# Optimization experiments

Measured on AMD Instinct MI355X. Metric: run time of the kernel, lower is better.

The kernel has to match this reference:

```python
import jax, jax.numpy as jnp
import numpy as np

B, C, H, W = 16, 512, 48, 48
INTER = 64  # C // reduction


def setup_inputs() -> dict:
    key = jax.random.key(0)
    k1, k2, k3, k4, k5 = jax.random.split(key, 5)
    s = 0.05
    return {
        "x": jax.random.normal(k1, (B, C, H, W), dtype=jnp.float32),
        "Wq": jax.random.normal(k2, (INTER, C), dtype=jnp.float32) * s,
        "Wk": jax.random.normal(k3, (INTER, C), dtype=jnp.float32) * s,
        "Wv": jax.random.normal(k4, (C, C), dtype=jnp.float32) * s,
        "gamma": jax.random.normal(k5, (1,), dtype=jnp.float32),
    }


def reference(x, Wq, Wk, Wv, gamma):
    b, c, h, w = x.shape
    n = h * w
    xf = x.reshape(b, c, n)                       # (B, C, N)
    # 1x1 convs == channel-mixing GEMMs
    q = jnp.einsum("ic,bcn->bin", Wq, xf)         # (B, inter, N)
    k = jnp.einsum("ic,bcn->bin", Wk, xf)         # (B, inter, N)
    v = jnp.einsum("oc,bcn->bon", Wv, xf)         # (B, C, N)
    # attn[b, n, m] = q[b, :, n] . k[b, :, m]; softmax over m
    attn = jnp.einsum("bin,bim->bnm", q, k)       # (B, N, N)
    attn = jax.nn.softmax(attn, axis=-1)
    # out[b, c, n] = sum_m v[b, c, m] * attn[b, n, m]
    out = jnp.einsum("bcm,bnm->bcn", v, attn).reshape(b, c, h, w)
    return gamma[0] * out + x
```

## Files before the change

### kernel.cpp

```cpp
#include <hip/hip_runtime.h>

#define BATCH 16
#define CHN   512
#define INTER 64
#define NPIX  2304

typedef _Float16 f16;
typedef _Float16 f16x8 __attribute__((ext_vector_type(8)));
typedef _Float16 f16x4 __attribute__((ext_vector_type(4)));
typedef short    s16x8 __attribute__((ext_vector_type(8)));
typedef float    f32x16 __attribute__((ext_vector_type(16)));

#define XT_OFF   ((size_t)0)
#define QT_OFF   ((size_t)37748736)
#define KT_OFF   ((size_t)42467328)
#define VB_OFF   ((size_t)47185920)
#define WHQ_OFF  ((size_t)84934656)
#define WHK_OFF  ((size_t)85000192)
#define WHV_OFF  ((size_t)85065728)

__device__ inline unsigned short f2bf(float f) {
    unsigned int u = __float_as_uint(f);
    unsigned int r = (u + 0x7FFFu + ((u >> 16) & 1u)) >> 16;
    return (unsigned short)r;
}

__device__ inline unsigned pack_bf16(float a, float b) {
    unsigned ua = __float_as_uint(a) + 0x8000u;
    unsigned ub = __float_as_uint(b) + 0x8000u;
    return __builtin_amdgcn_perm(ub, ua, 0x07060302u);
}

__device__ inline void swap32(unsigned x, unsigned y, unsigned& nx, unsigned& ny, int lh) {
#if __has_builtin(__builtin_amdgcn_permlane32_swap)
    auto r = __builtin_amdgcn_permlane32_swap(x, y, false, false);
    nx = r[0]; ny = r[1];
#else
    const unsigned xs = (unsigned)__shfl_xor((int)x, 32, 64);
    const unsigned ys = (unsigned)__shfl_xor((int)y, 32, 64);
    nx = lh ? ys : x;
    ny = lh ? y  : xs;
#endif
}

__global__ __launch_bounds__(256) void convert_x_kernel(
    const float* __restrict__ x, f16* __restrict__ xT)
{
    const int n0 = blockIdx.x * 64;
    const int c0 = blockIdx.y * 64;
    const int b  = blockIdx.z;
    const int t  = threadIdx.x;

    __shared__ float tile[64][65];

    {
        const int cr   = t >> 2;
        const int ncol = (t & 3) * 16;
        const float* src = x + ((size_t)b * CHN + (size_t)(c0 + cr)) * NPIX + n0 + ncol;
        #pragma unroll
        for (int u = 0; u < 4; ++u) {
            const float4 v4 = *(const float4*)(src + u * 4);
            tile[cr][ncol + u * 4 + 0] = v4.x;
            tile[cr][ncol + u * 4 + 1] = v4.y;
            tile[cr][ncol + u * 4 + 2] = v4.z;
            tile[cr][ncol + u * 4 + 3] = v4.w;
        }
    }
    __syncthreads();
    #pragma unroll
    for (int r = 0; r < 2; ++r) {
        const int id = t + r * 256;
        const int n  = id >> 3;
        const int cg = id & 7;
        f16x8 o;
        #pragma unroll
        for (int j = 0; j < 8; ++j) o[j] = (f16)tile[cg * 8 + j][n];
        *(f16x8*)(xT + ((size_t)b * NPIX + (size_t)(n0 + n)) * CHN + c0 + cg * 8) = o;
    }
}

__global__ __launch_bounds__(256) void convert_w_kernel(
    const float* __restrict__ Wq, const float* __restrict__ Wk,
    const float* __restrict__ Wv, f16* __restrict__ whq,
    f16* __restrict__ whk, f16* __restrict__ whv)
{
    const int which = blockIdx.y;
    const float* src; f16* dst; int count;
    if (which == 0)      { src = Wq; dst = whq; count = 64 * 512; }
    else if (which == 1) { src = Wk; dst = whk; count = 64 * 512; }
    else                 { src = Wv; dst = whv; count = 512 * 512; }
    const int i = (blockIdx.x * 256 + threadIdx.x) * 4;
    if (i < count) {
        const float4 v4 = *(const float4*)(src + i);
        f16x4 o;
        o[0] = (f16)v4.x; o[1] = (f16)v4.y; o[2] = (f16)v4.z; o[3] = (f16)v4.w;
        *(f16x4*)(dst + i) = o;
    }
}

__global__ __launch_bounds__(256, 2) void proj_kernel(
    const f16* __restrict__ xT, const f16* __restrict__ whq,
    const f16* __restrict__ whk, const f16* __restrict__ whv,
    f16* __restrict__ qTo, f16* __restrict__ kTo,
    unsigned short* __restrict__ vout)
{
    const int nt = blockIdx.x;
    const int rt = blockIdx.y;
    const int b  = blockIdx.z;
    const int t  = threadIdx.x;
    const int wave = t >> 6, lane = t & 63;
    const int row = lane & 31, lh = lane >> 5;

    __shared__ f16 wsm[128][72];
    __shared__ f16 xs[128][72];

    f32x16 acc[4];
    #pragma unroll
    for (int s = 0; s < 4; ++s)
        #pragma unroll
        for (int r = 0; r < 16; ++r) acc[s][r] = 0.0f;

    for (int c0 = 0; c0 < CHN; c0 += 64) {
        __syncthreads();
        #pragma unroll
        for (int r = 0; r < 4; ++r) {
            const int id = t + r * 256;
            const int co = id >> 3, cg = id & 7;
            const f16* src;
            if (rt == 0) src = (co < 64) ? (whq + (size_t)co * CHN)
                                         : (whk + (size_t)(co - 64) * CHN);
            else         src = whv + (size_t)((rt - 1) * 128 + co) * CHN;
            *(f16x8*)&wsm[co][cg * 8] = *(const f16x8*)(src + c0 + cg * 8);
        }
        #pragma unroll
        for (int r = 0; r < 4; ++r) {
            const int id = t + r * 256;
            const int n = id >> 3, cg = id & 7;
            *(f16x8*)&xs[n][cg * 8] =
                *(const f16x8*)(xT + ((size_t)b * NPIX + (size_t)(nt * 128 + n)) * CHN + c0 + cg * 8);
        }
        __syncthreads();

        #pragma unroll
        for (int kk = 0; kk < 64; kk += 16) {
            const f16x8 bf = *(const f16x8*)&xs[wave * 32 + row][kk + lh * 8];
            #pragma unroll
            for (int cs = 0; cs < 4; ++cs) {
                const f16x8 af = *(const f16x8*)&wsm[cs * 32 + row][kk + lh * 8];
                acc[cs] = __builtin_amdgcn_mfma_f32_32x32x16_f16(af, bf, acc[cs], 0, 0, 0);
            }
        }
    }

    const int n = nt * 128 + wave * 32 + row;
    if (rt == 0) {
        #pragma unroll
        for (int cs = 0; cs < 4; ++cs)
            #pragma unroll
            for (int r = 0; r < 16; ++r) {
                const int i = cs * 32 + (r & 3) + 8 * (r >> 2) + 4 * lh;
                const f16 val = (f16)acc[cs][r];
                if (i < 64) qTo[((size_t)b * NPIX + n) * INTER + i] = val;
                else        kTo[((size_t)b * NPIX + n) * INTER + i - 64] = val;
            }
    } else {
        #pragma unroll
        for (int cs = 0; cs < 4; ++cs)
            #pragma unroll
            for (int r = 0; r < 16; ++r) {
                const int c = (rt - 1) * 128 + cs * 32 + (r & 3) + 8 * (r >> 2) + 4 * lh;
                vout[((size_t)b * CHN + c) * NPIX + n] = f2bf(acc[cs][r]);
            }
    }
}

__global__ __launch_bounds__(256, 3) void attn_kernel(
    const float* __restrict__ x, const float* __restrict__ gamma,
    const f16* __restrict__ qT, const f16* __restrict__ kT,
    const unsigned short* __restrict__ vglob, float* __restrict__ out)
{
    const int nt = blockIdx.x;
    const int cq = blockIdx.y;
    const int b  = blockIdx.z;
    const int t  = threadIdx.x;
    const int wave = t >> 6, lane = t & 63;
    const int row = lane & 31, lh = lane >> 5;

    __shared__ short vbuf[2][128 * 64];
    __shared__ f16   kbuf[2][64 * 64];

    const unsigned short* vq = vglob + ((size_t)b * CHN + (size_t)cq * 128) * NPIX;
    const f16* kb = kT + (size_t)b * NPIX * INTER;

    const int vcr = t >> 3;
    const int vmc = t & 7;
    const int kmm = t >> 3;
    const int kic = t & 7;

    const int xorv = row & 7;

    f16x8 qf[4];
    {
        const f16* qrow = qT + ((size_t)b * NPIX
                          + (size_t)(nt * 128 + wave * 32 + row)) * INTER + lh * 8;
        #pragma unroll
        for (int k0 = 0; k0 < 4; ++k0) qf[k0] = *(const f16x8*)(qrow + k0 * 16);
    }

    #pragma unroll
    for (int j = 0; j < 4; ++j) {
        const int cr = vcr + j * 32;
        const s16x8 g = *(const s16x8*)(vq + (size_t)cr * NPIX + vmc * 8);
        *(s16x8*)&vbuf[0][cr * 64 + ((vmc ^ (cr & 7)) * 8)] = g;
    }
    #pragma unroll
    for (int j = 0; j < 2; ++j) {
        const int mm = kmm + j * 32;
        const f16x8 g = *(const f16x8*)(kb + (size_t)mm * INTER + kic * 8);
        *(f16x8*)&kbuf[0][mm * 64 + ((kic ^ (mm & 7)) * 8)] = g;
    }
    __syncthreads();

    f32x16 accv[4];
    #pragma unroll
    for (int s = 0; s < 4; ++s)
        #pragma unroll
        for (int r = 0; r < 16; ++r) accv[s][r] = 0.0f;

    float lrun = 0.0f;
    union PB { unsigned u[4]; s16x8 v; };

    for (int it = 0; it < NPIX / 64; ++it) {
        const int cur = it & 1, nxt = cur ^ 1;
        const int m1 = (it < NPIX / 64 - 1) ? (it + 1) * 64 : 0;

        s16x8 vg[4]; f16x8 kg[2];
        #pragma unroll
        for (int j = 0; j < 4; ++j)
            vg[j] = *(const s16x8*)(vq + (size_t)(vcr + j * 32) * NPIX + m1 + vmc * 8);
        #pragma unroll
        for (int j = 0; j < 2; ++j)
            kg[j] = *(const f16x8*)(kb + (size_t)(m1 + kmm + j * 32) * INTER + kic * 8);

        PB pb[4];
        #pragma unroll
        for (int mh = 0; mh < 2; ++mh) {
            f32x16 sacc;
            #pragma unroll
            for (int r = 0; r < 16; ++r) sacc[r] = 0.0f;
            #pragma unroll
            for (int k0 = 0; k0 < 4; ++k0) {
                const f16x8 af = *(const f16x8*)&kbuf[cur][(mh * 32 + row) * 64
                                    + (((k0 * 2 + lh) ^ xorv) * 8)];
                sacc = __builtin_amdgcn_mfma_f32_32x32x16_f16(af, qf[k0], sacc, 0, 0, 0);
            }
            float lp = 0.0f;
            unsigned pg[8];
            #pragma unroll
            for (int tt = 0; tt < 8; ++tt) {
                const float p0 = __expf(sacc[2 * tt + 0]);
                const float p1 = __expf(sacc[2 * tt + 1]);
                lp += p0 + p1;
                pg[tt] = pack_bf16(p0, p1);
            }
            lrun += lp;
            #pragma unroll
            for (int half = 0; half < 2; ++half)
                #pragma unroll
                for (int p = 0; p < 2; ++p) {
                    unsigned nx, ny;
                    swap32(pg[half * 4 + p], pg[half * 4 + 2 + p], nx, ny, lh);
                    pb[2 * mh + half].u[p]     = nx;
                    pb[2 * mh + half].u[p + 2] = ny;
                }
        }

        #pragma unroll
        for (int j = 0; j < 4; ++j) {
            const int cr = vcr + j * 32;
            *(s16x8*)&vbuf[nxt][cr * 64 + ((vmc ^ (cr & 7)) * 8)] = vg[j];
        }
        #pragma unroll
        for (int j = 0; j < 2; ++j) {
            const int mm = kmm + j * 32;
            *(f16x8*)&kbuf[nxt][mm * 64 + ((kic ^ (mm & 7)) * 8)] = kg[j];
        }

        #pragma unroll
        for (int cs = 0; cs < 4; ++cs)
            #pragma unroll
            for (int kk = 0; kk < 4; ++kk) {
                const s16x8 va = *(const s16x8*)&vbuf[cur][(cs * 32 + row) * 64
                                    + (((kk * 2 + lh) ^ xorv) * 8)];
                accv[cs] = __builtin_amdgcn_mfma_f32_32x32x16_bf16(
                    va, pb[kk].v, accv[cs], 0, 0, 0);
            }

        __syncthreads();
    }

    const float g = gamma[0];
    const float linv = 1.0f / (lrun + __shfl_xor(lrun, 32, 64));
    const int n = nt * 128 + wave * 32 + row;

    #pragma unroll
    for (int cs = 0; cs < 4; ++cs)
        #pragma unroll
        for (int r = 0; r < 16; ++r) {
            const int c = cq * 128 + cs * 32 + (r & 3) + 8 * (r >> 2) + 4 * lh;
            const size_t idx = ((size_t)b * CHN + c) * NPIX + n;
            out[idx] = g * accv[cs][r] * linv + x[idx];
        }
}

extern "C" void kernel_launch(void* const* d_in, const int* in_sizes, int n_in,
                              void* d_out, int out_size, void* d_ws, size_t ws_size,
                              hipStream_t stream) {
    (void)in_sizes; (void)n_in; (void)out_size; (void)ws_size;
    const float* x     = (const float*)d_in[0];
    const float* Wq    = (const float*)d_in[1];
    const float* Wk    = (const float*)d_in[2];
    const float* Wv    = (const float*)d_in[3];
    const float* gamma = (const float*)d_in[4];
    float* out = (float*)d_out;
    char* ws = (char*)d_ws;

    f16* xT  = (f16*)(ws + XT_OFF);
    f16* qTp = (f16*)(ws + QT_OFF);
    f16* kTp = (f16*)(ws + KT_OFF);
    unsigned short* vb = (unsigned short*)(ws + VB_OFF);
    f16* whq = (f16*)(ws + WHQ_OFF);
    f16* whk = (f16*)(ws + WHK_OFF);
    f16* whv = (f16*)(ws + WHV_OFF);

    convert_x_kernel<<<dim3(36, 8, 16), 256, 0, stream>>>(x, xT);
    convert_w_kernel<<<dim3(256, 3, 1), 256, 0, stream>>>(Wq, Wk, Wv, whq, whk, whv);
    proj_kernel<<<dim3(18, 5, 16), 256, 0, stream>>>(xT, whq, whk, whv, qTp, kTp, vb);
    attn_kernel<<<dim3(18, 4, 16), 256, 0, stream>>>(x, gamma, qTp, kTp, vb, out);
}
```

Baseline: 359.9 us.

## Stage projection epilogue through LDS, fold log2e into Q, single-buffer K in attention

The projection kernel now writes its accumulators into shared memory and then issues coalesced 16-byte global stores for q/k/v, replacing scattered 2-byte stores. Q is pre-scaled by log2(e) so the attention softmax can use the hardware exp2 instruction instead of __expf. The attention kernel single-buffers the K tile, adding an extra barrier per iteration, to cut LDS use and raise the occupancy hint from 3 to 4 blocks per CU. The extra barrier serialises the score phase against the K tile store, which may cost some overlap.

After: 688.2 us. 1.91x slower.

```diff
diff --git a/kernel.cpp b/kernel.cpp
--- a/kernel.cpp
+++ b/kernel.cpp
@@ -19,6 +19,8 @@
 #define WHK_OFF  ((size_t)85000192)
 #define WHV_OFF  ((size_t)85065728)
 
+#define LOG2E 1.4426950408889634f
+
 __device__ inline unsigned short f2bf(float f) {
     unsigned int u = __float_as_uint(f);
     unsigned int r = (u + 0x7FFFu + ((u >> 16) & 1u)) >> 16;
@@ -29,6 +31,20 @@
     unsigned ua = __float_as_uint(a) + 0x8000u;
     unsigned ub = __float_as_uint(b) + 0x8000u;
     return __builtin_amdgcn_perm(ub, ua, 0x07060302u);
+}
+
+__device__ inline unsigned pack_f16(float a, float b) {
+    f16 ha = (f16)a, hb = (f16)b;
+    unsigned short ua = *(unsigned short*)&ha, ub = *(unsigned short*)&hb;
+    return (unsigned)ua | ((unsigned)ub << 16);
+}
+
+__device__ inline float exp2_fast(float x) {
+#if __has_builtin(__builtin_amdgcn_exp2f)
+    return __builtin_amdgcn_exp2f(x);
+#else
+    float r; asm("v_exp_f32 %0, %1" : "=v"(r) : "v"(x)); return r;
+#endif
 }
 
 __device__ inline void swap32(unsigned x, unsigned y, unsigned& nx, unsigned& ny, int lh) {
@@ -111,8 +127,9 @@
     const int wave = t >> 6, lane = t & 63;
     const int row = lane & 31, lh = lane >> 5;
 
-    __shared__ f16 wsm[128][72];
-    __shared__ f16 xs[128][72];
+    __shared__ f16 smem[2 * 128 * 72];
+    f16 (*wsm)[72] = (f16(*)[72])smem;
+    f16 (*xs)[72]  = (f16(*)[72])(smem + 128 * 72);
 
     f32x16 acc[4];
     #pragma unroll
@@ -152,29 +169,56 @@
         }
     }
 
-    const int n = nt * 128 + wave * 32 + row;
+    __syncthreads();
+    unsigned short* eb = (unsigned short*)smem;
+    const int nl = wave * 32 + row;
+
     if (rt == 0) {
         #pragma unroll
+        for (int cs = 0; cs < 4; ++cs) {
+            const float sc = (cs < 2) ? LOG2E : 1.0f;
+            #pragma unroll
+            for (int tp = 0; tp < 8; ++tp) {
+                const int r = tp * 2;
+                const int i = cs * 32 + (r & 3) + 8 * (r >> 2) + 4 * lh;
+                *(unsigned*)&eb[nl * 130 + i] =
+                    pack_f16(acc[cs][r] * sc, acc[cs][r + 1] * sc);
+            }
+        }
+    } else {
+        #pragma unroll
         for (int cs = 0; cs < 4; ++cs)
             #pragma unroll
             for (int r = 0; r < 16; ++r) {
-                const int i = cs * 32 + (r & 3) + 8 * (r >> 2) + 4 * lh;
-                const f16 val = (f16)acc[cs][r];
-                if (i < 64) qTo[((size_t)b * NPIX + n) * INTER + i] = val;
-                else        kTo[((size_t)b * NPIX + n) * INTER + i - 64] = val;
-            }
-    } else {
-        #pragma unroll
-        for (int cs = 0; cs < 4; ++cs)
-            #pragma unroll
-            for (int r = 0; r < 16; ++r) {
-                const int c = (rt - 1) * 128 + cs * 32 + (r & 3) + 8 * (r >> 2) + 4 * lh;
-                vout[((size_t)b * CHN + c) * NPIX + n] = f2bf(acc[cs][r]);
-            }
-    }
-}
-
-__global__ __launch_bounds__(256, 3) void attn_kernel(
+                const int cl = cs * 32 + (r & 3) + 8 * (r >> 2) + 4 * lh;
+                eb[cl * 130 + nl] = f2bf(acc[cs][r]);
+            }
+    }
+    __syncthreads();
+
+    #pragma unroll
+    for (int u = 0; u < 8; ++u) {
+        const int id = t + u * 256;
+        const int rr = id >> 4;
+        const int ch = id & 15;
+        const unsigned short* src = &eb[rr * 130 + ch * 8];
+        s16x8 w;
+        #pragma unroll
+        for (int k = 0; k < 4; ++k)
+            ((unsigned*)&w)[k] = *(const unsigned*)(src + k * 2);
+        if (rt == 0) {
+            f16* dst = (ch < 8)
+                ? (qTo + ((size_t)b * NPIX + nt * 128 + rr) * INTER + ch * 8)
+                : (kTo + ((size_t)b * NPIX + nt * 128 + rr) * INTER + (ch - 8) * 8);
+            *(s16x8*)dst = w;
+        } else {
+            *(s16x8*)(vout + ((size_t)b * CHN + (size_t)((rt - 1) * 128 + rr)) * NPIX
+                      + nt * 128 + ch * 8) = w;
+        }
+    }
+}
+
+__global__ __launch_bounds__(256, 4) void attn_kernel(
     const float* __restrict__ x, const float* __restrict__ gamma,
     const f16* __restrict__ qT, const f16* __restrict__ kT,
     const unsigned short* __restrict__ vglob, float* __restrict__ out)
@@ -187,7 +231,7 @@
     const int row = lane & 31, lh = lane >> 5;
 
     __shared__ short vbuf[2][128 * 64];
-    __shared__ f16   kbuf[2][64 * 64];
+    __shared__ f16   kbuf[64 * 64];
 
     const unsigned short* vq = vglob + ((size_t)b * CHN + (size_t)cq * 128) * NPIX;
     const f16* kb = kT + (size_t)b * NPIX * INTER;
@@ -217,7 +261,7 @@
     for (int j = 0; j < 2; ++j) {
         const int mm = kmm + j * 32;
         const f16x8 g = *(const f16x8*)(kb + (size_t)mm * INTER + kic * 8);
-        *(f16x8*)&kbuf[0][mm * 64 + ((kic ^ (mm & 7)) * 8)] = g;
+        *(f16x8*)&kbuf[mm * 64 + ((kic ^ (mm & 7)) * 8)] = g;
     }
     __syncthreads();
 
@@ -242,7 +286,7 @@
         for (int j = 0; j < 2; ++j)
             kg[j] = *(const f16x8*)(kb + (size_t)(m1 + kmm + j * 32) * INTER + kic * 8);
 
-        PB pb[4];
+        union PB pb[4];
         #pragma unroll
         for (int mh = 0; mh < 2; ++mh) {
             f32x16 sacc;
@@ -250,7 +294,7 @@
             for (int r = 0; r < 16; ++r) sacc[r] = 0.0f;
             #pragma unroll
             for (int k0 = 0; k0 < 4; ++k0) {
-                const f16x8 af = *(const f16x8*)&kbuf[cur][(mh * 32 + row) * 64
+                const f16x8 af = *(const f16x8*)&kbuf[(mh * 32 + row) * 64
                                     + (((k0 * 2 + lh) ^ xorv) * 8)];
                 sacc = __builtin_amdgcn_mfma_f32_32x32x16_f16(af, qf[k0], sacc, 0, 0, 0);
             }
@@ -258,8 +302,8 @@
             unsigned pg[8];
             #pragma unroll
             for (int tt = 0; tt < 8; ++tt) {
-                const float p0 = __expf(sacc[2 * tt + 0]);
-                const float p1 = __expf(sacc[2 * tt + 1]);
+                const float p0 = exp2_fast(sacc[2 * tt + 0]);
+                const float p1 = exp2_fast(sacc[2 * tt + 1]);
                 lp += p0 + p1;
                 pg[tt] = pack_bf16(p0, p1);
             }
@@ -275,6 +319,8 @@
                 }
         }
 
+        __syncthreads();
+
         #pragma unroll
         for (int j = 0; j < 4; ++j) {
             const int cr = vcr + j * 32;
@@ -283,7 +329,7 @@
         #pragma unroll
         for (int j = 0; j < 2; ++j) {
             const int mm = kmm + j * 32;
-            *(f16x8*)&kbuf[nxt][mm * 64 + ((kic ^ (mm & 7)) * 8)] = kg[j];
+            *(f16x8*)&kbuf[mm * 64 + ((kic ^ (mm & 7)) * 8)] = kg[j];
         }
 
         #pragma unroll
```
